# Optimization experiments

Measured on AMD Instinct MI355X. Metric: run time of the kernel, lower is better.

The kernel has to match this reference:

```python
import jax, jax.numpy as jnp
import numpy as np

B = 256            # number of graphs
N_NODES = 512      # nodes per graph
D = 128            # embedding_dim = hidden_dim
NUM_EDGE_CLASSES = 8
N_TOTAL = B * N_NODES
N_EDGES = N_TOTAL * 8   # avg degree 8
EDGES_DIM = N_NODES * (N_NODES - 1) // 2


def _ln(x, g, b):
    m = jnp.mean(x, axis=-1, keepdims=True)
    v = jnp.var(x, axis=-1, keepdims=True)
    return (x - m) * jax.lax.rsqrt(v + 1e-5) * g + b


def _mlp_ln(x, W1, b1, g, be, W2, b2):
    # MLP(input,hidden,output, n_hidden_layers=1, add_layer_norm=True):
    # Linear -> LayerNorm -> ReLU -> Linear
    return jax.nn.relu(_ln(x @ W1 + b1, g, be)) @ W2 + b2


def setup_inputs() -> dict:
    key = jax.random.key(0)
    ks = jax.random.split(key, 12)
    s = 1.0 / np.sqrt(D)
    return {
        "node_features": jax.random.randint(ks[0], (N_TOTAL, 1), 0, N_NODES),
        "edge_index": jax.random.randint(ks[1], (2, N_EDGES), 0, N_TOTAL),
        "batch_ptr": jnp.arange(B + 1, dtype=jnp.int32) * N_NODES,
        "emb": jax.random.normal(ks[2], (N_NODES, D), jnp.float32) * 0.02,
        "gin_W1": jax.random.normal(ks[3], (D, D), jnp.float32) * s,
        "gin_b1": jnp.zeros((D,), jnp.float32),
        "gin_g1": jnp.ones((D,), jnp.float32),
        "gin_be1": jnp.zeros((D,), jnp.float32),
        "gin_W2": jax.random.normal(ks[4], (D, D), jnp.float32) * s,
        "gin_b2": jnp.zeros((D,), jnp.float32),
        "post_W1": jax.random.normal(ks[5], (D, D), jnp.float32) * s,
        "post_b1": jnp.zeros((D,), jnp.float32),
        "post_W2": jax.random.normal(ks[6], (D, D), jnp.float32) * s,
        "post_b2": jnp.zeros((D,), jnp.float32),
        "norm_g": jnp.ones((D,), jnp.float32),
        "norm_b": jnp.zeros((D,), jnp.float32),
        "exit_W1": jax.random.normal(ks[7], (D, D), jnp.float32) * s,
        "exit_b1": jnp.zeros((D,), jnp.float32),
        "exit_g": jnp.ones((D,), jnp.float32),
        "exit_be": jnp.zeros((D,), jnp.float32),
        "exit_W2": jax.random.normal(ks[8], (D, 1), jnp.float32) * s,
        "exit_b2": jnp.zeros((1,), jnp.float32),
    }


def reference(node_features, edge_index, batch_ptr, emb,
              gin_W1, gin_b1, gin_g1, gin_be1, gin_W2, gin_b2,
              post_W1, post_b1, post_W2, post_b2,
              norm_g, norm_b,
              exit_W1, exit_b1, exit_g, exit_be, exit_W2, exit_b2):
    # node embedding lookup
    x = emb[node_features.squeeze(-1)]                      # [N_total, D]

    # single GIN conv layer (eps=0): MLP(x + sum_{j in N(i)} x_j)
    src, dst = edge_index[0], edge_index[1]
    agg = jax.ops.segment_sum(x[src], dst, num_segments=N_TOTAL)
    h = _mlp_ln(x + agg, gin_W1, gin_b1, gin_g1, gin_be1, gin_W2, gin_b2)
    # post-conv Sequential(Linear, ReLU, Linear)
    h = jax.nn.relu(h @ post_W1 + post_b1) @ post_W2 + post_b2
    # i == 0: no residual; then LayerNorm
    x = _ln(h, norm_g, norm_b)                              # [N_total, D]

    # segment mean via cumsum (faithful to _group_mean)
    cs = jnp.concatenate([jnp.zeros((1, D), x.dtype), jnp.cumsum(x, axis=0)], 0)
    sizes = (batch_ptr[1:] - batch_ptr[:-1]).astype(x.dtype)
    means = (cs[batch_ptr[1:]] - cs[batch_ptr[:-1]]) / sizes[:, None]  # [B, D]

    exit_action = _mlp_ln(means, exit_W1, exit_b1, exit_g, exit_be,
                          exit_W2, exit_b2).squeeze(-1)     # [B]

    # per-graph pairwise dot products, upper-triangular gather
    xb = x.reshape(B, N_NODES, D)
    scores = jnp.einsum('bnf,bmf->bnm', xb, xb) / jnp.sqrt(
        jnp.asarray(D, x.dtype))                            # [B, n, n]
    iu, ju = jnp.triu_indices(N_NODES, k=1)
    edge_actions = scores[:, iu, ju]                        # [B, EDGES_DIM]

    # action_type: index 1 = ADD_EDGE, 2 = EXIT (GraphActionType assumption)
    action_type = (jnp.zeros((B, 3), x.dtype)
                   .at[:, 1].set(1.0 - exit_action)
                   .at[:, 2].set(exit_action))
    edge_class = jnp.zeros((B, NUM_EDGE_CLASSES), x.dtype)
    node_class = jnp.zeros((B, 1), x.dtype)
    return (action_type, edge_class, node_class, edge_actions)
```

## Files before the change

kernel.cpp:

```cpp
#include <hip/hip_runtime.h>
#include <hip/hip_bf16.h>

#define NBATCH 256
#define NNODES 512
#define DIM    128
#define NTOT   (NBATCH*NNODES)
#define NEDGE  (NTOT*8)
#define EPB    130816
#define CAP    32

typedef __attribute__((ext_vector_type(8))) short  short8;
typedef __attribute__((ext_vector_type(4))) float  f32x4;

__device__ __forceinline__ unsigned short f2bf(float f){
  unsigned u = __builtin_bit_cast(unsigned, f);
  unsigned r = u + 0x7FFFu + ((u >> 16) & 1u);
  return (unsigned short)(r >> 16);
}

__global__ __launch_bounds__(256) void k_prep(
    const float* __restrict__ emb, const float* __restrict__ W1,
    unsigned short* __restrict__ embW1,
    const float* __restrict__ W2, const float* __restrict__ P1,
    const float* __restrict__ P2, unsigned short* __restrict__ wswz,
    int* __restrict__ cnt)
{
  const int tid = threadIdx.x;
  const int blk = blockIdx.x;
  __shared__ float er[2][DIM];
  if (blk < 256) {
    const int half = tid >> 7, c = tid & 127;
    const int r = blk*2 + half;
    er[half][c] = emb[r*DIM + c];
    __syncthreads();
    float acc = 0.f;
    #pragma unroll 8
    for (int k = 0; k < DIM; ++k) acc = fmaf(er[half][k], W1[k*DIM + c], acc);
    embW1[r*DIM + c] = f2bf(acc);
  } else if (blk < 448) {
    int idx = (blk - 256)*256 + tid;
    int s = idx >> 14, rem = idx & 16383;
    int ks = rem >> 12, n = (rem >> 9) & 7, lane = (rem >> 3) & 63, j = rem & 7;
    int lg = lane >> 4, l15 = lane & 15;
    int k = ks*32 + lg*8 + j, c = n*16 + l15;
    const float* src = (s == 0) ? W2 : ((s == 1) ? P1 : P2);
    wswz[idx] = f2bf(src[k*DIM + c]);
  } else {
    cnt[(blk - 448)*256 + tid] = 0;
  }
}

__global__ __launch_bounds__(256) void k_edges(const int* __restrict__ ei,
                                               const int* __restrict__ nf,
                                               int* __restrict__ cnt,
                                               unsigned short* __restrict__ slots){
  const int base = (blockIdx.x >> 3)*4096 + threadIdx.x;
  const int r    = blockIdx.x & 7;
  #pragma unroll
  for (int it = 0; it < 16; ++it) {
    const int e = base + it*256;
    const int d = ei[NEDGE + e];
    if ((d >> 14) == r) {
      const int s = ei[e];
      const int v = nf[s];
      const int pos = atomicAdd(&cnt[d], 1);
      if (pos < CAP) slots[(size_t)d*CAP + pos] = (unsigned short)v;
    }
  }
}

__global__ __launch_bounds__(1024, 1) void k_mega(
    const unsigned short* __restrict__ embW1, const int* __restrict__ nf,
    const int* __restrict__ cnt, const unsigned short* __restrict__ slots,
    const float* __restrict__ b1, const float* __restrict__ g1,
    const float* __restrict__ be1,
    const unsigned short* __restrict__ wswz,
    const float* __restrict__ b2,  const float* __restrict__ pb1, const float* __restrict__ pb2,
    const float* __restrict__ ng,  const float* __restrict__ nbv,
    const float* __restrict__ eW1, const float* __restrict__ eb1,
    const float* __restrict__ eg,  const float* __restrict__ ebe,
    const float* __restrict__ eW2, const float* __restrict__ eb2,
    float* __restrict__ out)
{
  __shared__ unsigned short X[512][136];
  __shared__ float gpart[16][128];
  __shared__ float mrow[128];
  __shared__ int   tq;
  const int tid   = threadIdx.x;
  const int bb    = blockIdx.x;
  const int nbase = bb * NNODES;
  if (tid == 0) tq = 0;

  {
    const int part = tid & 15;
    const short8* base8 = (const short8*)embW1;
    #pragma unroll 1
    for (int pass = 0; pass < 8; ++pass) {
      const int lnode = pass*64 + (tid >> 4);
      const int node  = nbase + lnode;
      const int self = nf[node];
      int m = cnt[node]; if (m > CAP) m = CAP;
      const unsigned short* sl = slots + (size_t)node*CAP;
      const uint4 sv0 = *(const uint4*)(sl);
      const uint4 sv1 = *(const uint4*)(sl + 8);
      const uint4 sv2 = *(const uint4*)(sl + 16);
      unsigned sw[12] = {sv0.x,sv0.y,sv0.z,sv0.w, sv1.x,sv1.y,sv1.z,sv1.w,
                         sv2.x,sv2.y,sv2.z,sv2.w};
      float a[8];
      {
        const float4* bp = (const float4*)(b1 + part*8);
        float4 x = bp[0], y = bp[1];
        a[0]=x.x; a[1]=x.y; a[2]=x.z; a[3]=x.w;
        a[4]=y.x; a[5]=y.y; a[6]=y.z; a[7]=y.w;
      }
#define ACC8(V) { _Pragma("unroll") \
      for (int i_ = 0; i_ < 8; ++i_) { \
        unsigned uu = ((unsigned)(unsigned short)(V)[i_]) << 16; \
        a[i_] += __builtin_bit_cast(float, uu); } }
      {
        short8 t0 = base8[(size_t)self*16 + part];
        short8 t[8];
        #pragma unroll
        for (int e = 0; e < 8; ++e) {
          unsigned id = (sw[e >> 1] >> ((e & 1)*16)) & 0xffffu;
          int idx = (e < m) ? (int)id : self;
          t[e] = base8[(size_t)idx*16 + part];
        }
        ACC8(t0)
        #pragma unroll
        for (int e = 0; e < 8; ++e) if (e < m) ACC8(t[e])
      }
      if (m > 8) {
        short8 t[8];
        #pragma unroll
        for (int e = 0; e < 8; ++e) {
          unsigned id = (sw[4 + (e >> 1)] >> ((e & 1)*16)) & 0xffffu;
          int idx = (e + 8 < m) ? (int)id : self;
          t[e] = base8[(size_t)idx*16 + part];
        }
        #pragma unroll
        for (int e = 0; e < 8; ++e) if (e + 8 < m) ACC8(t[e])
      }
      if (m > 16) {
        short8 t[8];
        #pragma unroll
        for (int e = 0; e < 8; ++e) {
          unsigned id = (sw[8 + (e >> 1)] >> ((e & 1)*16)) & 0xffffu;
          int idx = (e + 16 < m) ? (int)id : self;
          t[e] = base8[(size_t)idx*16 + part];
        }
        #pragma unroll
        for (int e = 0; e < 8; ++e) if (e + 16 < m) ACC8(t[e])
      }
      for (int e = 24; e < m; ++e) {
        short8 t = base8[(size_t)sl[e]*16 + part];
        ACC8(t)
      }
      float s = 0.f, qs = 0.f;
      #pragma unroll
      for (int i = 0; i < 8; ++i) { s += a[i]; qs += a[i]*a[i]; }
      #pragma unroll
      for (int msk = 1; msk < 16; msk <<= 1) {
        s  += __shfl_xor(s,  msk, 64);
        qs += __shfl_xor(qs, msk, 64);
      }
      const float mean = s * (1.f/128.f);
      const float var  = qs * (1.f/128.f) - mean*mean;
      const float rs   = rsqrtf(var + 1e-5f);
      const float4* gp = (const float4*)(g1  + part*8);
      const float4* ep = (const float4*)(be1 + part*8);
      float4 g0 = gp[0], g1v = gp[1], e0 = ep[0], e1v = ep[1];
      float gg[8] = {g0.x,g0.y,g0.z,g0.w, g1v.x,g1v.y,g1v.z,g1v.w};
      float eb[8] = {e0.x,e0.y,e0.z,e0.w, e1v.x,e1v.y,e1v.z,e1v.w};
      float v[8];
      #pragma unroll
      for (int i = 0; i < 8; ++i)
        v[i] = fmaxf((a[i] - mean)*rs*gg[i] + eb[i], 0.f);
      uint4 pk;
      pk.x = (unsigned)f2bf(v[0]) | ((unsigned)f2bf(v[1]) << 16);
      pk.y = (unsigned)f2bf(v[2]) | ((unsigned)f2bf(v[3]) << 16);
      pk.z = (unsigned)f2bf(v[4]) | ((unsigned)f2bf(v[5]) << 16);
      pk.w = (unsigned)f2bf(v[6]) | ((unsigned)f2bf(v[7]) << 16);
      *(uint4*)&X[lnode][part*8] = pk;
    }
  }
  __syncthreads();

  const int wave = tid >> 6, lane = tid & 63;
  const int l15 = lane & 15, lg = lane >> 4;
  const short8* ws8 = (const short8*)wswz;
  const float PRESCL = 0.29730177875068026f;
  float pc[8];
  #pragma unroll
  for (int n = 0; n < 8; ++n) pc[n] = 0.f;

  #pragma unroll
  for (int s = 0; s < 3; ++s) {
    f32x4 acc[2][8];
    #pragma unroll
    for (int p2 = 0; p2 < 2; ++p2)
      #pragma unroll
      for (int n = 0; n < 8; ++n) acc[p2][n] = (f32x4){0.f,0.f,0.f,0.f};
    #pragma unroll
    for (int ks = 0; ks < 4; ++ks) {
      short8 bf[8];
      #pragma unroll
      for (int n = 0; n < 8; ++n) bf[n] = ws8[s*2048 + ks*512 + n*64 + lane];
      #pragma unroll
      for (int p2 = 0; p2 < 2; ++p2) {
        short8 af = *(const short8*)&X[p2*256 + wave*16 + l15][ks*32 + lg*8];
        #pragma unroll
        for (int n = 0; n < 8; ++n)
          acc[p2][n] = __builtin_amdgcn_mfma_f32_16x16x32_bf16(af, bf[n], acc[p2][n], 0, 0, 0);
      }
    }
    if (s < 2) {
      const float* bias = (s == 0) ? b2 : pb1;
      float bv[8];
      #pragma unroll
      for (int n = 0; n < 8; ++n) bv[n] = bias[n*16 + l15];
      #pragma unroll
      for (int p2 = 0; p2 < 2; ++p2)
        #pragma unroll
        for (int n = 0; n < 8; ++n)
          #pragma unroll
          for (int q = 0; q < 4; ++q) {
            float v = acc[p2][n][q] + bv[n];
            if (s == 1) v = fmaxf(v, 0.f);
            X[p2*256 + wave*16 + lg*4 + q][n*16 + l15] = f2bf(v);
          }
    } else {
      float bv[8], gc[8], bc[8];
      #pragma unroll
      for (int n = 0; n < 8; ++n) {
        bv[n] = pb2[n*16 + l15];
        gc[n] = ng [n*16 + l15];
        bc[n] = nbv[n*16 + l15];
      }
      #pragma unroll
      for (int p2 = 0; p2 < 2; ++p2) {
        float sr[4] = {0,0,0,0}, qr[4] = {0,0,0,0};
        #pragma unroll
        for (int n = 0; n < 8; ++n)
          #pragma unroll
          for (int q = 0; q < 4; ++q) {
            float v = acc[p2][n][q] + bv[n];
            acc[p2][n][q] = v;
            sr[q] += v; qr[q] += v*v;
          }
        #pragma unroll
        for (int msk = 1; msk < 16; msk <<= 1)
          #pragma unroll
          for (int q = 0; q < 4; ++q) {
            sr[q] += __shfl_xor(sr[q], msk, 64);
            qr[q] += __shfl_xor(qr[q], msk, 64);
          }
        float mean[4], rs[4];
        #pragma unroll
        for (int q = 0; q < 4; ++q) {
          mean[q] = sr[q]*(1.f/128.f);
          float var = qr[q]*(1.f/128.f) - mean[q]*mean[q];
          rs[q] = rsqrtf(var + 1e-5f);
        }
        #pragma unroll
        for (int n = 0; n < 8; ++n)
          #pragma unroll
          for (int q = 0; q < 4; ++q) {
            float xo = (acc[p2][n][q] - mean[q])*rs[q]*gc[n] + bc[n];
            X[p2*256 + wave*16 + lg*4 + q][n*16 + l15] = f2bf(xo * PRESCL);
            pc[n] += xo;
          }
      }
    }
  }
  #pragma unroll
  for (int n = 0; n < 8; ++n) {
    pc[n] += __shfl_xor(pc[n], 16, 64);
    pc[n] += __shfl_xor(pc[n], 32, 64);
  }
  if (lg == 0) {
    #pragma unroll
    for (int n = 0; n < 8; ++n) gpart[wave][n*16 + l15] = pc[n];
  }
  __syncthreads();

  if (wave == 0) {
    const int c0 = lane, c1 = lane + 64;
    float m0 = 0.f, m1 = 0.f;
    #pragma unroll
    for (int w = 0; w < 16; ++w) { m0 += gpart[w][c0]; m1 += gpart[w][c1]; }
    mrow[c0] = m0 * (1.f/512.f);
    mrow[c1] = m1 * (1.f/512.f);
    float u0 = eb1[c0], u1 = eb1[c1];
    #pragma unroll 8
    for (int k = 0; k < DIM; ++k) {
      const float mk = mrow[k];
      u0 = fmaf(mk, eW1[k*DIM + c0], u0);
      u1 = fmaf(mk, eW1[k*DIM + c1], u1);
    }
    float s2 = u0 + u1, q2 = u0*u0 + u1*u1;
    #pragma unroll
    for (int msk = 1; msk < 64; msk <<= 1) {
      s2 += __shfl_xor(s2, msk, 64); q2 += __shfl_xor(q2, msk, 64);
    }
    const float mean = s2*(1.f/128.f);
    const float var  = q2*(1.f/128.f) - mean*mean;
    const float rs   = rsqrtf(var + 1e-5f);
    float a0 = fmaxf((u0 - mean)*rs*eg[c0] + ebe[c0], 0.f);
    float a1 = fmaxf((u1 - mean)*rs*eg[c1] + ebe[c1], 0.f);
    float p = a0*eW2[c0] + a1*eW2[c1];
    #pragma unroll
    for (int msk = 1; msk < 64; msk <<= 1) p += __shfl_xor(p, msk, 64);
    if (lane == 0) {
      float e = p + eb2[0];
      out[bb*3 + 0] = 0.f;
      out[bb*3 + 1] = 1.f - e;
      out[bb*3 + 2] = e;
    }
  }
  if (wave == 1) {
    if (lane < 8)   out[768 + bb*8 + lane] = 0.f;
    if (lane == 8)  out[2816 + bb] = 0.f;
  }

  float* ea = out + 3072 + (size_t)bb*EPB;
  for (;;) {
    int task = 0;
    if (lane == 0) task = atomicAdd(&tq, 1);
    task = __shfl(task, 0, 64);
    if (task >= 80) break;
    const int p  = task >> 3, rg = task & 7;
    const int ti = (int)((0x3221110000ULL >> (p*4)) & 0xF);
    const int tj = (int)((0x3323213210ULL >> (p*4)) & 0xF);
    const bool diag = (ti == tj);
    const int nlo = diag ? rg : 0;

    f32x4 acc[8];
    #pragma unroll
    for (int n = 0; n < 8; ++n) acc[n] = (f32x4){0,0,0,0};
    #pragma unroll
    for (int ks = 0; ks < 4; ++ks) {
      const int k0 = ks*32 + lg*8;
      short8 afrag = *(const short8*)&X[ti*128 + rg*16 + l15][k0];
      #pragma unroll
      for (int n = 0; n < 8; ++n) {
        if (n >= nlo) {
          short8 bfrag = *(const short8*)&X[tj*128 + n*16 + l15][k0];
          acc[n] = __builtin_amdgcn_mfma_f32_16x16x32_bf16(afrag, bfrag, acc[n], 0, 0, 0);
        }
      }
    }
    const int gib = ti*128 + rg*16 + lg*4;
    int rb[4];
    #pragma unroll
    for (int q = 0; q < 4; ++q) {
      const int gi = gib + q;
      rb[q] = gi*511 - ((gi*(gi-1)) >> 1) - gi - 1;
    }
    #pragma unroll
    for (int n = 0; n < 8; ++n) {
      if (n < nlo) continue;
      const int gj = tj*128 + n*16 + l15;
      if (!diag || n > rg) {
        #pragma unroll
        for (int q = 0; q < 4; ++q) ea[rb[q] + gj] = acc[n][q];
      } else {
        #pragma unroll
        for (int q = 0; q < 4; ++q)
          if (gj > gib + q) ea[rb[q] + gj] = acc[n][q];
      }
    }
  }
}

extern "C" void kernel_launch(void* const* d_in, const int* in_sizes, int n_in,
                              void* d_out, int out_size, void* d_ws, size_t ws_size,
                              hipStream_t stream) {
  const int*   nf   = (const int*)d_in[0];
  const int*   ei   = (const int*)d_in[1];
  const float* emb  = (const float*)d_in[3];
  const float* gW1  = (const float*)d_in[4];
  const float* gb1  = (const float*)d_in[5];
  const float* gg1  = (const float*)d_in[6];
  const float* gbe1 = (const float*)d_in[7];
  const float* gW2  = (const float*)d_in[8];
  const float* gb2  = (const float*)d_in[9];
  const float* pW1  = (const float*)d_in[10];
  const float* pb1  = (const float*)d_in[11];
  const float* pW2  = (const float*)d_in[12];
  const float* pb2  = (const float*)d_in[13];
  const float* ng   = (const float*)d_in[14];
  const float* nb   = (const float*)d_in[15];
  const float* eW1  = (const float*)d_in[16];
  const float* eb1  = (const float*)d_in[17];
  const float* eg   = (const float*)d_in[18];
  const float* ebe  = (const float*)d_in[19];
  const float* eW2  = (const float*)d_in[20];
  const float* eb2  = (const float*)d_in[21];
  float* out = (float*)d_out;

  char* ws = (char*)d_ws;
  unsigned short* embW1 = (unsigned short*)ws;
  unsigned short* wswz  = (unsigned short*)(ws + 262144);
  int*            cnt   = (int*)(ws + 360448);
  unsigned short* slots = (unsigned short*)(ws + 884736);
  if (ws_size < 9273344) return;

  k_prep  <<<960,  256, 0, stream>>>(emb, gW1, embW1, gW2, pW1, pW2, wswz, cnt);
  k_edges <<<2048, 256, 0, stream>>>(ei, nf, cnt, slots);
  k_mega  <<<256, 1024, 0, stream>>>(embW1, nf, cnt, slots, gb1, gg1, gbe1,
                                     wswz, gb2, pb1, pb2, ng, nb,
                                     eW1, eb1, eg, ebe, eW2, eb2, out);
}
```

Measured before the change: 138.1 us.

## Transpose MLP MFMA operands for packed stores and pair row groups in pairwise tiles

The MLP stage swaps the MFMA A and B operands so each lane holds four consecutive output columns. Epilogue writes to LDS become packed 8-byte stores, and bias/gamma/beta load as float4. The LayerNorm row reduction shrinks to two cross-lane shuffles instead of a 16-lane butterfly. The pairwise score stage processes two 16-row groups per task, reusing each B fragment for two MFMAs and halving the task count. The launch bounds hint goes from 1 to 4 blocks per SM, which tightens register limits and may cause spills given the larger accumulator arrays, even though 1024-thread blocks with large LDS cannot actually co-reside.

```diff
diff --git a/kernel.cpp b/kernel.cpp
--- a/kernel.cpp
+++ b/kernel.cpp
@@ -69,7 +69,7 @@
   }
 }
 
-__global__ __launch_bounds__(1024, 1) void k_mega(
+__global__ __launch_bounds__(1024, 4) void k_mega(
     const unsigned short* __restrict__ embW1, const int* __restrict__ nf,
     const int* __restrict__ cnt, const unsigned short* __restrict__ slots,
     const float* __restrict__ b1, const float* __restrict__ g1,
@@ -190,9 +190,8 @@
   const int l15 = lane & 15, lg = lane >> 4;
   const short8* ws8 = (const short8*)wswz;
   const float PRESCL = 0.29730177875068026f;
-  float pc[8];
-  #pragma unroll
-  for (int n = 0; n < 8; ++n) pc[n] = 0.f;
+  const int xrow0 = wave*16 + l15;
+  const int cbase = lg*4;
 
   #pragma unroll
   for (int s = 0; s < 3; ++s) {
@@ -208,79 +207,85 @@
       for (int n = 0; n < 8; ++n) bf[n] = ws8[s*2048 + ks*512 + n*64 + lane];
       #pragma unroll
       for (int p2 = 0; p2 < 2; ++p2) {
-        short8 af = *(const short8*)&X[p2*256 + wave*16 + l15][ks*32 + lg*8];
+        short8 af = *(const short8*)&X[p2*256 + xrow0][ks*32 + lg*8];
         #pragma unroll
         for (int n = 0; n < 8; ++n)
-          acc[p2][n] = __builtin_amdgcn_mfma_f32_16x16x32_bf16(af, bf[n], acc[p2][n], 0, 0, 0);
+          acc[p2][n] = __builtin_amdgcn_mfma_f32_16x16x32_bf16(bf[n], af, acc[p2][n], 0, 0, 0);
       }
     }
     if (s < 2) {
       const float* bias = (s == 0) ? b2 : pb1;
-      float bv[8];
-      #pragma unroll
-      for (int n = 0; n < 8; ++n) bv[n] = bias[n*16 + l15];
       #pragma unroll
       for (int p2 = 0; p2 < 2; ++p2)
         #pragma unroll
-        for (int n = 0; n < 8; ++n)
+        for (int n = 0; n < 8; ++n) {
+          float4 bq = *(const float4*)(bias + n*16 + cbase);
+          float v0 = acc[p2][n][0] + bq.x, v1 = acc[p2][n][1] + bq.y;
+          float v2 = acc[p2][n][2] + bq.z, v3 = acc[p2][n][3] + bq.w;
+          if (s == 1) {
+            v0 = fmaxf(v0, 0.f); v1 = fmaxf(v1, 0.f);
+            v2 = fmaxf(v2, 0.f); v3 = fmaxf(v3, 0.f);
+          }
+          uint2 pk;
+          pk.x = (unsigned)f2bf(v0) | ((unsigned)f2bf(v1) << 16);
+          pk.y = (unsigned)f2bf(v2) | ((unsigned)f2bf(v3) << 16);
+          *(uint2*)&X[p2*256 + xrow0][n*16 + cbase] = pk;
+        }
+    } else {
+      float sr[2] = {0,0}, qr[2] = {0,0};
+      #pragma unroll
+      for (int p2 = 0; p2 < 2; ++p2)
+        #pragma unroll
+        for (int n = 0; n < 8; ++n) {
+          float4 bq = *(const float4*)(pb2 + n*16 + cbase);
           #pragma unroll
           for (int q = 0; q < 4; ++q) {
-            float v = acc[p2][n][q] + bv[n];
-            if (s == 1) v = fmaxf(v, 0.f);
-            X[p2*256 + wave*16 + lg*4 + q][n*16 + l15] = f2bf(v);
+            float v = acc[p2][n][q] + ((const float*)&bq)[q];
+            acc[p2][n][q] = v;
+            sr[p2] += v; qr[p2] += v*v;
           }
-    } else {
-      float bv[8], gc[8], bc[8];
+        }
+      #pragma unroll
+      for (int p2 = 0; p2 < 2; ++p2) {
+        sr[p2] += __shfl_xor(sr[p2], 16, 64);
+        sr[p2] += __shfl_xor(sr[p2], 32, 64);
+        qr[p2] += __shfl_xor(qr[p2], 16, 64);
+        qr[p2] += __shfl_xor(qr[p2], 32, 64);
+      }
+      float mean[2], rs[2];
+      #pragma unroll
+      for (int p2 = 0; p2 < 2; ++p2) {
+        mean[p2] = sr[p2]*(1.f/128.f);
+        float var = qr[p2]*(1.f/128.f) - mean[p2]*mean[p2];
+        rs[p2] = rsqrtf(var + 1e-5f);
+      }
       #pragma unroll
       for (int n = 0; n < 8; ++n) {
-        bv[n] = pb2[n*16 + l15];
-        gc[n] = ng [n*16 + l15];
-        bc[n] = nbv[n*16 + l15];
-      }
-      #pragma unroll
-      for (int p2 = 0; p2 < 2; ++p2) {
-        float sr[4] = {0,0,0,0}, qr[4] = {0,0,0,0};
-        #pragma unroll
-        for (int n = 0; n < 8; ++n)
+        float4 gq = *(const float4*)(ng  + n*16 + cbase);
+        float4 bq = *(const float4*)(nbv + n*16 + cbase);
+        float pcq[4] = {0,0,0,0};
+        #pragma unroll
+        for (int p2 = 0; p2 < 2; ++p2) {
+          float xo[4];
           #pragma unroll
           for (int q = 0; q < 4; ++q) {
-            float v = acc[p2][n][q] + bv[n];
-            acc[p2][n][q] = v;
-            sr[q] += v; qr[q] += v*v;
+            xo[q] = (acc[p2][n][q] - mean[p2])*rs[p2]*((const float*)&gq)[q]
+                    + ((const float*)&bq)[q];
+            pcq[q] += xo[q];
           }
+          uint2 pk;
+          pk.x = (unsigned)f2bf(xo[0]*PRESCL) | ((unsigned)f2bf(xo[1]*PRESCL) << 16);
+          pk.y = (unsigned)f2bf(xo[2]*PRESCL) | ((unsigned)f2bf(xo[3]*PRESCL) << 16);
+          *(uint2*)&X[p2*256 + xrow0][n*16 + cbase] = pk;
+        }
         #pragma unroll
         for (int msk = 1; msk < 16; msk <<= 1)
           #pragma unroll
-          for (int q = 0; q < 4; ++q) {
-            sr[q] += __shfl_xor(sr[q], msk, 64);
-            qr[q] += __shfl_xor(qr[q], msk, 64);
-          }
-        float mean[4], rs[4];
-        #pragma unroll
-        for (int q = 0; q < 4; ++q) {
-          mean[q] = sr[q]*(1.f/128.f);
-          float var = qr[q]*(1.f/128.f) - mean[q]*mean[q];
-          rs[q] = rsqrtf(var + 1e-5f);
-        }
-        #pragma unroll
-        for (int n = 0; n < 8; ++n)
-          #pragma unroll
-          for (int q = 0; q < 4; ++q) {
-            float xo = (acc[p2][n][q] - mean[q])*rs[q]*gc[n] + bc[n];
-            X[p2*256 + wave*16 + lg*4 + q][n*16 + l15] = f2bf(xo * PRESCL);
-            pc[n] += xo;
-          }
-      }
-    }
-  }
-  #pragma unroll
-  for (int n = 0; n < 8; ++n) {
-    pc[n] += __shfl_xor(pc[n], 16, 64);
-    pc[n] += __shfl_xor(pc[n], 32, 64);
-  }
-  if (lg == 0) {
-    #pragma unroll
-    for (int n = 0; n < 8; ++n) gpart[wave][n*16 + l15] = pc[n];
+          for (int q = 0; q < 4; ++q) pcq[q] += __shfl_xor(pcq[q], msk, 64);
+        if (l15 == 0)
+          *(float4*)&gpart[wave][n*16 + cbase] = make_float4(pcq[0],pcq[1],pcq[2],pcq[3]);
+      }
+    }
   }
   __syncthreads();
 
@@ -328,46 +333,57 @@
     int task = 0;
     if (lane == 0) task = atomicAdd(&tq, 1);
     task = __shfl(task, 0, 64);
-    if (task >= 80) break;
-    const int p  = task >> 3, rg = task & 7;
+    if (task >= 40) break;
+    const int p = task >> 2, rgp = task & 3;
     const int ti = (int)((0x3221110000ULL >> (p*4)) & 0xF);
     const int tj = (int)((0x3323213210ULL >> (p*4)) & 0xF);
     const bool diag = (ti == tj);
-    const int nlo = diag ? rg : 0;
-
-    f32x4 acc[8];
-    #pragma unroll
-    for (int n = 0; n < 8; ++n) acc[n] = (f32x4){0,0,0,0};
+    const int rg0 = rgp*2, rg1 = rgp*2 + 1;
+    const int nlo0 = diag ? rg0 : 0;
+
+    f32x4 acc[2][8];
+    #pragma unroll
+    for (int r = 0; r < 2; ++r)
+      #pragma unroll
+      for (int n = 0; n < 8; ++n) acc[r][n] = (f32x4){0,0,0,0};
     #pragma unroll
     for (int ks = 0; ks < 4; ++ks) {
       const int k0 = ks*32 + lg*8;
-      short8 afrag = *(const short8*)&X[ti*128 + rg*16 + l15][k0];
+      short8 a0 = *(const short8*)&X[ti*128 + rg0*16 + l15][k0];
+      short8 a1 = *(const short8*)&X[ti*128 + rg1*16 + l15][k0];
       #pragma unroll
       for (int n = 0; n < 8; ++n) {
-        if (n >= nlo) {
+        if (n >= nlo0) {
           short8 bfrag = *(const short8*)&X[tj*128 + n*16 + l15][k0];
-          acc[n] = __builtin_amdgcn_mfma_f32_16x16x32_bf16(afrag, bfrag, acc[n], 0, 0, 0);
-        }
-      }
-    }
-    const int gib = ti*128 + rg*16 + lg*4;
-    int rb[4];
-    #pragma unroll
-    for (int q = 0; q < 4; ++q) {
-      const int gi = gib + q;
-      rb[q] = gi*511 - ((gi*(gi-1)) >> 1) - gi - 1;
-    }
-    #pragma unroll
-    for (int n = 0; n < 8; ++n) {
-      if (n < nlo) continue;
-      const int gj = tj*128 + n*16 + l15;
-      if (!diag || n > rg) {
-        #pragma unroll
-        for (int q = 0; q < 4; ++q) ea[rb[q] + gj] = acc[n][q];
-      } else {
-        #pragma unroll
-        for (int q = 0; q < 4; ++q)
-          if (gj > gib + q) ea[rb[q] + gj] = acc[n][q];
+          acc[0][n] = __builtin_amdgcn_mfma_f32_16x16x32_bf16(a0, bfrag, acc[0][n], 0, 0, 0);
+          if (!diag || n >= rg1)
+            acc[1][n] = __builtin_amdgcn_mfma_f32_16x16x32_bf16(a1, bfrag, acc[1][n], 0, 0, 0);
+        }
+      }
+    }
+    #pragma unroll
+    for (int r = 0; r < 2; ++r) {
+      const int rg  = rgp*2 + r;
+      const int nlo = diag ? rg : 0;
+      const int gib = ti*128 + rg*16 + lg*4;
+      int rb[4];
+      #pragma unroll
+      for (int q = 0; q < 4; ++q) {
+        const int gi = gib + q;
+        rb[q] = gi*511 - ((gi*(gi-1)) >> 1) - gi - 1;
+      }
+      #pragma unroll
+      for (int n = 0; n < 8; ++n) {
+        if (n < nlo) continue;
+        const int gj = tj*128 + n*16 + l15;
+        if (!diag || n > rg) {
+          #pragma unroll
+          for (int q = 0; q < 4; ++q) ea[rb[q] + gj] = acc[r][n][q];
+        } else {
+          #pragma unroll
+          for (int q = 0; q < 4; ++q)
+            if (gj > gib + q) ea[rb[q] + gj] = acc[r][n][q];
+        }
       }
     }
   }
```

New measurement: 138.8 us, median of 2. About the same (+0.5%).
